# Performance work log

Hardware: AMD Instinct MI355X
Metric: run time of the kernel (lower is better)

The kernel has to match this reference:

```python
import jax, jax.numpy as jnp
import numpy as np

B, N, H, EMB, BOT = 32, 128, 64, 64, 64


def _node2edge(x):
    # x: (B, N, F) -> edges (B, N*N, 2F); edge e=i*N+j holds [x[j] (receiver), x[i] (sender)]
    b, n, f = x.shape
    recv = jnp.broadcast_to(x[:, None, :, :], (b, n, n, f))  # varies with j
    send = jnp.broadcast_to(x[:, :, None, :], (b, n, n, f))  # varies with i
    return jnp.concatenate([recv, send], axis=-1).reshape(b, n * n, 2 * f)


def _edge2node(e, n):
    # e: (B, N*N, F); receiver of edge i*N+j is j -> sum over i; divide by FEATURE dim (faithful to source)
    b, _, f = e.shape
    return e.reshape(b, n, n, f).sum(axis=1) / f


def _lin(x, w, b):
    return x @ w + b


def setup_inputs() -> dict:
    key = jax.random.key(0)
    ks = jax.random.split(key, 24)

    def w(k, i, o):
        return jax.random.normal(k, (i, o), jnp.float32) / np.sqrt(i)

    def bias(k, o):
        return jax.random.normal(k, (o,), jnp.float32) * 0.01

    return {
        "h_states": jax.random.normal(ks[0], (B, N, H), jnp.float32),
        "end_pos": jax.random.normal(ks[1], (B, N, 2), jnp.float32),
        "se_w": w(ks[2], 2, EMB), "se_b": bias(ks[3], EMB),
        "s1_w": w(ks[4], 2 * H + EMB, 128), "s1_b": bias(ks[5], 128),
        "s2_w": w(ks[6], 128, H), "s2_b": bias(ks[7], H),
        "n1_w": w(ks[8], H, 128), "n1_b": bias(ks[9], 128),
        "n2_w": w(ks[10], 128, H), "n2_b": bias(ks[11], H),
        "e1_w": w(ks[12], 2 * H, 128), "e1_b": bias(ks[13], 128),
        "e2_w": w(ks[14], 128, H), "e2_b": bias(ks[15], H),
        "f1_w": w(ks[16], H, 128), "f1_b": bias(ks[17], 128),
        "f2_w": w(ks[18], 128, BOT), "f2_b": bias(ks[19], BOT),
    }


def reference(h_states, end_pos, se_w, se_b, s1_w, s1_b, s2_w, s2_b,
              n1_w, n1_b, n2_w, n2_b, e1_w, e1_b, e2_w, e2_b,
              f1_w, f1_b, f2_w, f2_b):
    b, n, _ = h_states.shape
    # relative positions: pos[i] - pos[j] for edge i*N+j -> (B, N*N, 2)
    rel_pos = (end_pos[:, :, None, :] - end_pos[:, None, :, :]).reshape(b, n * n, 2)
    rel_emb = _lin(rel_pos, se_w, se_b)  # (B, N*N, EMB)

    edge_feat = jnp.concatenate([_node2edge(h_states), rel_emb], axis=-1)  # (B, N*N, 2H+EMB)
    # nmp_mlp_start: two linears, no activation (activation=None), dropout inert in eval
    edge_feat = _lin(_lin(edge_feat, s1_w, s1_b), s2_w, s2_b)  # (B, N*N, H)

    # nmp_layers=2 -> one (node mlp, edge mlp) pair, no activations
    node_feat = _lin(_lin(_edge2node(edge_feat, n), n1_w, n1_b), n2_w, n2_b)
    edge_feat = _lin(_lin(_node2edge(node_feat), e1_w, e1_b), e2_w, e2_b)

    # nmp_mlp_end: Linear -> ReLU -> Linear -> ReLU
    x = _edge2node(edge_feat, n)
    x = jax.nn.relu(_lin(x, f1_w, f1_b))
    x = jax.nn.relu(_lin(x, f2_w, f2_b))
    return x  # (B, N, BOT)
```

## Files before the change

### kernel.cpp

```cpp
#include <hip/hip_runtime.h>

enum : int {
  WS_A1  = 0,
  WS_B1  = 4096,
  WS_SE2 = 8192,
  WS_NW  = 12288,
  WS_D1  = 16384,
  WS_D2  = 20480,
  WS_K0  = 24576,
  WS_NB  = 24704,
  WS_D0  = 24768,
  WS_P1  = 24832,
  WS_P2  = 28928,
  WS_A2  = 37120,
  WS_K1  = 37248,
  WS_C2  = 37312,
  WS_H1  = 37440,
  WS_H2  = 45632,
  WS_H3  = 45888,
  WS_END = 49984
};

template<int N, int BS>
__device__ __forceinline__ void dot4row(const float* __restrict__ a, int as,
                                        const float* __restrict__ b, float c[4]){
  float c0=0.f,c1=0.f,c2=0.f,c3=0.f;
  #pragma unroll
  for (int k=0;k<N;++k){
    float bv = b[k*BS];
    c0 = fmaf(a[k],        bv, c0);
    c1 = fmaf(a[as+k],     bv, c1);
    c2 = fmaf(a[2*as+k],   bv, c2);
    c3 = fmaf(a[3*as+k],   bv, c3);
  }
  c[0]=c0;c[1]=c1;c[2]=c2;c[3]=c3;
}

template<int N, int BS>
__device__ __forceinline__ float dot1(const float* __restrict__ a, const float* __restrict__ b){
  float c = 0.f;
  #pragma unroll
  for (int k=0;k<N;++k) c = fmaf(a[k], b[k*BS], c);
  return c;
}

__global__ __launch_bounds__(256) void k_lvl0(
    const float* __restrict__ se_b,
    const float* __restrict__ s1_w, const float* __restrict__ s1_b,
    const float* __restrict__ s2_w,
    const float* __restrict__ n1_w, const float* __restrict__ n1_b,
    const float* __restrict__ n2_w, const float* __restrict__ n2_b,
    const float* __restrict__ e1_w, const float* __restrict__ e1_b,
    const float* __restrict__ e2_w, const float* __restrict__ e2_b,
    float* __restrict__ ws)
{
  int blk = blockIdx.x, t = threadIdx.x;
  if (blk < 24) {
    int which = blk >> 2, lb = blk & 3;
    int col = t & 63, row = lb * 16 + (t >> 6) * 4;
    const float* a; const float* b; float* o;
    switch (which) {
      case 0: a = s1_w + row * 128;         b = s2_w + col; o = ws + WS_A1;  break;
      case 1: a = s1_w + (64 + row) * 128;  b = s2_w + col; o = ws + WS_B1;  break;
      case 2: a = s1_w + (128 + row) * 128; b = s2_w + col; o = ws + WS_SE2; break;
      case 3: a = n1_w + row * 128;         b = n2_w + col; o = ws + WS_NW;  break;
      case 4: a = e1_w + row * 128;         b = e2_w + col; o = ws + WS_D1;  break;
      default:a = e1_w + (64 + row) * 128;  b = e2_w + col; o = ws + WS_D2;  break;
    }
    float c[4];
    dot4row<128, 64>(a, 128, b, c);
    #pragma unroll
    for (int i = 0; i < 4; ++i) o[(row + i) * 64 + col] = c[i];
  } else {
    if (t < 128) {
      ws[WS_K0 + t] = dot1<64, 128>(se_b, s1_w + 128 * 128 + t) + s1_b[t];
    } else if (t < 192) {
      int c = t - 128;
      ws[WS_NB + c] = dot1<128, 64>(n1_b, n2_w + c) + n2_b[c];
    } else {
      int c = t - 192;
      ws[WS_D0 + c] = 2.f * (dot1<128, 64>(e1_b, e2_w + c) + e2_b[c]);
    }
  }
}

__global__ __launch_bounds__(256) void k_lvl1(
    const float* __restrict__ se_w, const float* __restrict__ s2_w,
    const float* __restrict__ f1_w, float* __restrict__ ws)
{
  int blk = blockIdx.x, t = threadIdx.x;
  if (blk < 4) {
    int col = t & 63, row = blk * 16 + (t >> 6) * 4;
    float c[4];
    dot4row<64, 64>(ws + WS_A1 + row * 64, 64, ws + WS_NW + col, c);
    #pragma unroll
    for (int i = 0; i < 4; ++i) ws[WS_P1 + (row + i) * 64 + col] = c[i];
  } else if (blk < 12) {
    int c128 = t & 127, row = (blk - 4) * 8 + (t >> 7) * 4;
    float c[4];
    dot4row<64, 128>(ws + WS_D1 + row * 64, 64, f1_w + c128, c);
    #pragma unroll
    for (int i = 0; i < 4; ++i) ws[WS_P2 + (row + i) * 128 + c128] = c[i];
  } else {
    __shared__ float sA2[128];
    if (t < 128) {
      int r = t >> 6, c = t & 63;
      float v = dot1<64, 64>(se_w + r * 64, ws + WS_SE2 + c);
      sA2[t] = v;
      ws[WS_A2 + t] = v;
    } else if (t < 192) {
      int c = t - 128;
      ws[WS_K1 + c] = dot1<128, 64>(ws + WS_K0, s2_w + c);
    }
    __syncthreads();
    if (t < 128) {
      int r = t >> 6, c = t & 63;
      ws[WS_C2 + t] = -2.f * dot1<64, 64>(sA2 + r * 64, ws + WS_NW + c);
    }
  }
}

__global__ __launch_bounds__(256) void k_lvl2(
    const float* __restrict__ h, const float* __restrict__ pos,
    const float* __restrict__ s2_b, const float* __restrict__ f1_w,
    const float* __restrict__ f1_b, float* __restrict__ ws)
{
  int blk = blockIdx.x, t = threadIdx.x;
  if (blk < 8) {
    int c128 = t & 127, row = blk * 8 + (t >> 7) * 4;
    float c[4];
    dot4row<64, 128>(ws + WS_P1 + row * 64, 64, ws + WS_P2 + c128, c);
    #pragma unroll
    for (int i = 0; i < 4; ++i) ws[WS_H1 + (row + i) * 128 + c128] = 4.f * c[i];
    return;
  }
  if (blk == 8) {
    int r = t >> 7, c = t & 127;
    ws[WS_H2 + t] = 2.f * dot1<64, 128>(ws + WS_C2 + r * 64, ws + WS_P2 + c);
    return;
  }
  __shared__ float sX[64], sP[2], sv[64], sc3[64], sN[64], sg3[64], part[256];
  int b = blk - 9;
  { int k = t & 63, g = t >> 6; float s = 0.f;
    #pragma unroll 8
    for (int j = g * 32; j < g * 32 + 32; ++j) s += h[(b * 128 + j) * 64 + k];
    part[t] = s; }
  __syncthreads();
  if (t < 64) sX[t] = (part[t] + part[64 + t]) + (part[128 + t] + part[192 + t]);
  else if (t < 66) { int cc = t - 64; float s = 0.f;
    #pragma unroll 16
    for (int j = 0; j < 128; ++j) s += pos[(b * 128 + j) * 2 + cc];
    sP[cc] = s; }
  __syncthreads();
  if (t < 64) {
    float acc = dot1<64, 64>(sX, ws + WS_B1 + t);
    acc += sP[0] * ws[WS_A2 + t] + sP[1] * ws[WS_A2 + 64 + t];
    sv[t] = acc * (1.f / 64.f) + 2.f * ws[WS_K1 + t] + 2.f * s2_b[t];
  }
  __syncthreads();
  if (t < 64) {
    sc3[t] = dot1<64, 64>(sv, ws + WS_NW + t) + ws[WS_NB + t];
  }
  __syncthreads();
  if (t < 64) {
    float acc = 2.f * dot1<64, 64>(sX, ws + WS_P1 + t);
    sN[t] = acc + sP[0] * ws[WS_C2 + t] + sP[1] * ws[WS_C2 + 64 + t] + 128.f * sc3[t];
  }
  __syncthreads();
  if (t < 64) {
    float a1 = dot1<64, 64>(sc3, ws + WS_D1 + t);
    float a2 = dot1<64, 64>(sN, ws + WS_D2 + t);
    sg3[t] = 2.f * a1 + a2 * (1.f / 64.f) + ws[WS_D0 + t];
  }
  __syncthreads();
  if (t < 128) {
    ws[WS_H3 + b * 128 + t] = dot1<64, 128>(sg3, f1_w + t) + f1_b[t];
  }
}

__global__ __launch_bounds__(256) void k_main(
    const float* __restrict__ h, const float* __restrict__ pos,
    const float* __restrict__ f2_w, const float* __restrict__ f2_b,
    const float* __restrict__ ws, float* __restrict__ out)
{
  __shared__ __align__(16) float lH1[64 * 128];
  __shared__ __align__(16) float lH2[2 * 128];
  __shared__ float lh3[128], lf2b[64];
  __shared__ __align__(16) float lx[16 * 64];
  __shared__ float lp[16 * 2];
  __shared__ __align__(16) float lh1[16 * 128];
  int blk = blockIdx.x, t = threadIdx.x;
  int b = blk >> 3, j0 = (blk & 7) * 16;
  for (int i = t; i < 2048; i += 256) ((float4*)lH1)[i] = ((const float4*)(ws + WS_H1))[i];
  for (int i = t; i < 64; i += 256) ((float4*)lH2)[i] = ((const float4*)(ws + WS_H2))[i];
  if (t < 128) lh3[t] = ws[WS_H3 + b * 128 + t];
  if (t < 64) lf2b[t] = f2_b[t];
  { ((float4*)lx)[t] = ((const float4*)(h + (size_t)(b * 128 + j0) * 64))[t]; }
  if (t < 32) lp[t] = pos[(b * 128 + j0) * 2 + t];
  __syncthreads();
  {
    int d = t & 127, g = t >> 7, n0 = g * 8;
    float acc[8];
    #pragma unroll
    for (int i = 0; i < 8; ++i)
      acc[i] = lh3[d] + lp[(n0 + i) * 2] * lH2[d] + lp[(n0 + i) * 2 + 1] * lH2[128 + d];
    #pragma unroll 4
    for (int k = 0; k < 64; k += 4) {
      float h0 = lH1[k * 128 + d], h1v = lH1[(k + 1) * 128 + d],
            h2v = lH1[(k + 2) * 128 + d], h3v = lH1[(k + 3) * 128 + d];
      #pragma unroll
      for (int i = 0; i < 8; ++i) {
        float4 xv = *(const float4*)&lx[(n0 + i) * 64 + k];
        acc[i] = fmaf(xv.x, h0, fmaf(xv.y, h1v, fmaf(xv.z, h2v, fmaf(xv.w, h3v, acc[i]))));
      }
    }
    #pragma unroll
    for (int i = 0; i < 8; ++i) lh1[(n0 + i) * 128 + d] = fmaxf(acc[i], 0.f);
  }
  __syncthreads();
  {
    int d = t & 63, g = t >> 6, n0 = g * 4;
    float acc[4];
    #pragma unroll
    for (int i = 0; i < 4; ++i) acc[i] = lf2b[d];
    #pragma unroll 4
    for (int k = 0; k < 128; k += 4) {
      float f0 = f2_w[k * 64 + d], f1v = f2_w[(k + 1) * 64 + d],
            f2v = f2_w[(k + 2) * 64 + d], f3v = f2_w[(k + 3) * 64 + d];
      #pragma unroll
      for (int i = 0; i < 4; ++i) {
        float4 hv = *(const float4*)&lh1[(n0 + i) * 128 + k];
        acc[i] = fmaf(hv.x, f0, fmaf(hv.y, f1v, fmaf(hv.z, f2v, fmaf(hv.w, f3v, acc[i]))));
      }
    }
    #pragma unroll
    for (int i = 0; i < 4; ++i)
      out[(size_t)(b * 128 + j0 + n0 + i) * 64 + d] = fmaxf(acc[i], 0.f);
  }
}

extern "C" void kernel_launch(void* const* d_in, const int* in_sizes, int n_in,
                              void* d_out, int out_size, void* d_ws, size_t ws_size,
                              hipStream_t stream) {
  const float* h    = (const float*)d_in[0];
  const float* pos  = (const float*)d_in[1];
  const float* se_w = (const float*)d_in[2];
  const float* se_b = (const float*)d_in[3];
  const float* s1_w = (const float*)d_in[4];
  const float* s1_b = (const float*)d_in[5];
  const float* s2_w = (const float*)d_in[6];
  const float* s2_b = (const float*)d_in[7];
  const float* n1_w = (const float*)d_in[8];
  const float* n1_b = (const float*)d_in[9];
  const float* n2_w = (const float*)d_in[10];
  const float* n2_b = (const float*)d_in[11];
  const float* e1_w = (const float*)d_in[12];
  const float* e1_b = (const float*)d_in[13];
  const float* e2_w = (const float*)d_in[14];
  const float* e2_b = (const float*)d_in[15];
  const float* f1_w = (const float*)d_in[16];
  const float* f1_b = (const float*)d_in[17];
  const float* f2_w = (const float*)d_in[18];
  const float* f2_b = (const float*)d_in[19];
  float* ws = (float*)d_ws;
  float* out = (float*)d_out;

  hipLaunchKernelGGL(k_lvl0, dim3(25), dim3(256), 0, stream,
                     se_b, s1_w, s1_b, s2_w, n1_w, n1_b, n2_w, n2_b,
                     e1_w, e1_b, e2_w, e2_b, ws);
  hipLaunchKernelGGL(k_lvl1, dim3(13), dim3(256), 0, stream, se_w, s2_w, f1_w, ws);
  hipLaunchKernelGGL(k_lvl2, dim3(41), dim3(256), 0, stream, h, pos, s2_b, f1_w, f1_b, ws);
  hipLaunchKernelGGL(k_main, dim3(256), dim3(256), 0, stream, h, pos, f2_w, f2_b, ws, out);
}
```

Baseline: 32.91 us.

## Collapse three weight-folding launches into one prep kernel via vector chains

Replaces the three dependent precompute kernels with a single kernel. The first 32 blocks build the folded H1/H2 weight products column by column, each as a chain of matrix-vector products through the weights. The remaining 32 blocks compute the per-batch H3 vector by propagating through the layers directly instead of using precomposed 64x64 products. This removes two kernel launches and their dependency bubbles, at the cost of more serial per-block work and uncoalesced weight reads (threads stride rows of e2_w/n2_w/s2_w/e1_w/n1_w/s1_w) within each block.

```diff
diff --git a/kernel.cpp b/kernel.cpp
--- a/kernel.cpp
+++ b/kernel.cpp
@@ -1,180 +1,184 @@
 #include <hip/hip_runtime.h>
 
 enum : int {
-  WS_A1  = 0,
-  WS_B1  = 4096,
-  WS_SE2 = 8192,
-  WS_NW  = 12288,
-  WS_D1  = 16384,
-  WS_D2  = 20480,
-  WS_K0  = 24576,
-  WS_NB  = 24704,
-  WS_D0  = 24768,
-  WS_P1  = 24832,
-  WS_P2  = 28928,
-  WS_A2  = 37120,
-  WS_K1  = 37248,
-  WS_C2  = 37312,
-  WS_H1  = 37440,
-  WS_H2  = 45632,
-  WS_H3  = 45888,
-  WS_END = 49984
+  WS_H1 = 0,
+  WS_H2 = 8192,
+  WS_H3 = 8448,
+  WS_END = 12544
 };
 
-template<int N, int BS>
-__device__ __forceinline__ void dot4row(const float* __restrict__ a, int as,
-                                        const float* __restrict__ b, float c[4]){
-  float c0=0.f,c1=0.f,c2=0.f,c3=0.f;
-  #pragma unroll
-  for (int k=0;k<N;++k){
-    float bv = b[k*BS];
-    c0 = fmaf(a[k],        bv, c0);
-    c1 = fmaf(a[as+k],     bv, c1);
-    c2 = fmaf(a[2*as+k],   bv, c2);
-    c3 = fmaf(a[3*as+k],   bv, c3);
-  }
-  c[0]=c0;c[1]=c1;c[2]=c2;c[3]=c3;
-}
-
-template<int N, int BS>
-__device__ __forceinline__ float dot1(const float* __restrict__ a, const float* __restrict__ b){
-  float c = 0.f;
-  #pragma unroll
-  for (int k=0;k<N;++k) c = fmaf(a[k], b[k*BS], c);
-  return c;
-}
-
-__global__ __launch_bounds__(256) void k_lvl0(
-    const float* __restrict__ se_b,
+__global__ __launch_bounds__(256) void k_prep(
+    const float* __restrict__ h, const float* __restrict__ pos,
+    const float* __restrict__ se_w, const float* __restrict__ se_b,
     const float* __restrict__ s1_w, const float* __restrict__ s1_b,
-    const float* __restrict__ s2_w,
+    const float* __restrict__ s2_w, const float* __restrict__ s2_b,
     const float* __restrict__ n1_w, const float* __restrict__ n1_b,
     const float* __restrict__ n2_w, const float* __restrict__ n2_b,
     const float* __restrict__ e1_w, const float* __restrict__ e1_b,
     const float* __restrict__ e2_w, const float* __restrict__ e2_b,
+    const float* __restrict__ f1_w, const float* __restrict__ f1_b,
     float* __restrict__ ws)
 {
   int blk = blockIdx.x, t = threadIdx.x;
-  if (blk < 24) {
-    int which = blk >> 2, lb = blk & 3;
-    int col = t & 63, row = lb * 16 + (t >> 6) * 4;
-    const float* a; const float* b; float* o;
-    switch (which) {
-      case 0: a = s1_w + row * 128;         b = s2_w + col; o = ws + WS_A1;  break;
-      case 1: a = s1_w + (64 + row) * 128;  b = s2_w + col; o = ws + WS_B1;  break;
-      case 2: a = s1_w + (128 + row) * 128; b = s2_w + col; o = ws + WS_SE2; break;
-      case 3: a = n1_w + row * 128;         b = n2_w + col; o = ws + WS_NW;  break;
-      case 4: a = e1_w + row * 128;         b = e2_w + col; o = ws + WS_D1;  break;
-      default:a = e1_w + (64 + row) * 128;  b = e2_w + col; o = ws + WS_D2;  break;
-    }
-    float c[4];
-    dot4row<128, 64>(a, 128, b, c);
-    #pragma unroll
-    for (int i = 0; i < 4; ++i) o[(row + i) * 64 + col] = c[i];
+  if (blk < 32) {
+    __shared__ float wv[4][128];
+    __shared__ float uv[4][64];
+    int g = t >> 6, lane = t & 63, c = blk * 4 + g;
+    { float a0 = 0.f, a1 = 0.f;
+      #pragma unroll
+      for (int k = 0; k < 64; ++k) {
+        float f = f1_w[k * 128 + c];
+        a0 = fmaf(e2_w[lane * 64 + k], f, a0);
+        a1 = fmaf(e2_w[(lane + 64) * 64 + k], f, a1);
+      }
+      wv[g][lane] = a0; wv[g][lane + 64] = a1; }
+    __syncthreads();
+    { float a = 0.f;
+      #pragma unroll
+      for (int m = 0; m < 128; ++m) a = fmaf(e1_w[lane * 128 + m], wv[g][m], a);
+      uv[g][lane] = a; }
+    __syncthreads();
+    { float b0 = 0.f, b1 = 0.f;
+      #pragma unroll
+      for (int k = 0; k < 64; ++k) {
+        float u = uv[g][k];
+        b0 = fmaf(n2_w[lane * 64 + k], u, b0);
+        b1 = fmaf(n2_w[(lane + 64) * 64 + k], u, b1);
+      }
+      wv[g][lane] = b0; wv[g][lane + 64] = b1; }
+    __syncthreads();
+    { float a = 0.f;
+      #pragma unroll
+      for (int m = 0; m < 128; ++m) a = fmaf(n1_w[lane * 128 + m], wv[g][m], a);
+      uv[g][lane] = a; }
+    __syncthreads();
+    { float b0 = 0.f, b1 = 0.f;
+      #pragma unroll
+      for (int k = 0; k < 64; ++k) {
+        float u = uv[g][k];
+        b0 = fmaf(s2_w[lane * 64 + k], u, b0);
+        b1 = fmaf(s2_w[(lane + 64) * 64 + k], u, b1);
+      }
+      wv[g][lane] = b0; wv[g][lane + 64] = b1; }
+    __syncthreads();
+    { float a = 0.f, z = 0.f;
+      #pragma unroll
+      for (int m = 0; m < 128; ++m) {
+        float w = wv[g][m];
+        a = fmaf(s1_w[lane * 128 + m], w, a);
+        z = fmaf(s1_w[(128 + lane) * 128 + m], w, z);
+      }
+      ws[WS_H1 + lane * 128 + c] = 4.f * a;
+      float r0 = se_w[lane] * z, r1 = se_w[64 + lane] * z;
+      #pragma unroll
+      for (int m = 1; m < 64; m <<= 1) {
+        r0 += __shfl_xor(r0, m, 64);
+        r1 += __shfl_xor(r1, m, 64);
+      }
+      if (lane == 0) { ws[WS_H2 + c] = -4.f * r0; ws[WS_H2 + 128 + c] = -4.f * r1; } }
   } else {
-    if (t < 128) {
-      ws[WS_K0 + t] = dot1<64, 128>(se_b, s1_w + 128 * 128 + t) + s1_b[t];
-    } else if (t < 192) {
-      int c = t - 128;
-      ws[WS_NB + c] = dot1<128, 64>(n1_b, n2_w + c) + n2_b[c];
-    } else {
-      int c = t - 192;
-      ws[WS_D0 + c] = 2.f * (dot1<128, 64>(e1_b, e2_w + c) + e2_b[c]);
-    }
-  }
-}
-
-__global__ __launch_bounds__(256) void k_lvl1(
-    const float* __restrict__ se_w, const float* __restrict__ s2_w,
-    const float* __restrict__ f1_w, float* __restrict__ ws)
-{
-  int blk = blockIdx.x, t = threadIdx.x;
-  if (blk < 4) {
-    int col = t & 63, row = blk * 16 + (t >> 6) * 4;
-    float c[4];
-    dot4row<64, 64>(ws + WS_A1 + row * 64, 64, ws + WS_NW + col, c);
-    #pragma unroll
-    for (int i = 0; i < 4; ++i) ws[WS_P1 + (row + i) * 64 + col] = c[i];
-  } else if (blk < 12) {
-    int c128 = t & 127, row = (blk - 4) * 8 + (t >> 7) * 4;
-    float c[4];
-    dot4row<64, 128>(ws + WS_D1 + row * 64, 64, f1_w + c128, c);
-    #pragma unroll
-    for (int i = 0; i < 4; ++i) ws[WS_P2 + (row + i) * 128 + c128] = c[i];
-  } else {
-    __shared__ float sA2[128];
-    if (t < 128) {
-      int r = t >> 6, c = t & 63;
-      float v = dot1<64, 64>(se_w + r * 64, ws + WS_SE2 + c);
-      sA2[t] = v;
-      ws[WS_A2 + t] = v;
-    } else if (t < 192) {
-      int c = t - 128;
-      ws[WS_K1 + c] = dot1<128, 64>(ws + WS_K0, s2_w + c);
-    }
-    __syncthreads();
-    if (t < 128) {
-      int r = t >> 6, c = t & 63;
-      ws[WS_C2 + t] = -2.f * dot1<64, 64>(sA2 + r * 64, ws + WS_NW + c);
-    }
-  }
-}
-
-__global__ __launch_bounds__(256) void k_lvl2(
-    const float* __restrict__ h, const float* __restrict__ pos,
-    const float* __restrict__ s2_b, const float* __restrict__ f1_w,
-    const float* __restrict__ f1_b, float* __restrict__ ws)
-{
-  int blk = blockIdx.x, t = threadIdx.x;
-  if (blk < 8) {
-    int c128 = t & 127, row = blk * 8 + (t >> 7) * 4;
-    float c[4];
-    dot4row<64, 128>(ws + WS_P1 + row * 64, 64, ws + WS_P2 + c128, c);
-    #pragma unroll
-    for (int i = 0; i < 4; ++i) ws[WS_H1 + (row + i) * 128 + c128] = 4.f * c[i];
-    return;
-  }
-  if (blk == 8) {
-    int r = t >> 7, c = t & 127;
-    ws[WS_H2 + t] = 2.f * dot1<64, 128>(ws + WS_C2 + r * 64, ws + WS_P2 + c);
-    return;
-  }
-  __shared__ float sX[64], sP[2], sv[64], sc3[64], sN[64], sg3[64], part[256];
-  int b = blk - 9;
-  { int k = t & 63, g = t >> 6; float s = 0.f;
-    #pragma unroll 8
-    for (int j = g * 32; j < g * 32 + 32; ++j) s += h[(b * 128 + j) * 64 + k];
-    part[t] = s; }
-  __syncthreads();
-  if (t < 64) sX[t] = (part[t] + part[64 + t]) + (part[128 + t] + part[192 + t]);
-  else if (t < 66) { int cc = t - 64; float s = 0.f;
-    #pragma unroll 16
-    for (int j = 0; j < 128; ++j) s += pos[(b * 128 + j) * 2 + cc];
-    sP[cc] = s; }
-  __syncthreads();
-  if (t < 64) {
-    float acc = dot1<64, 64>(sX, ws + WS_B1 + t);
-    acc += sP[0] * ws[WS_A2 + t] + sP[1] * ws[WS_A2 + 64 + t];
-    sv[t] = acc * (1.f / 64.f) + 2.f * ws[WS_K1 + t] + 2.f * s2_b[t];
-  }
-  __syncthreads();
-  if (t < 64) {
-    sc3[t] = dot1<64, 64>(sv, ws + WS_NW + t) + ws[WS_NB + t];
-  }
-  __syncthreads();
-  if (t < 64) {
-    float acc = 2.f * dot1<64, 64>(sX, ws + WS_P1 + t);
-    sN[t] = acc + sP[0] * ws[WS_C2 + t] + sP[1] * ws[WS_C2 + 64 + t] + 128.f * sc3[t];
-  }
-  __syncthreads();
-  if (t < 64) {
-    float a1 = dot1<64, 64>(sc3, ws + WS_D1 + t);
-    float a2 = dot1<64, 64>(sN, ws + WS_D2 + t);
-    sg3[t] = 2.f * a1 + a2 * (1.f / 64.f) + ws[WS_D0 + t];
-  }
-  __syncthreads();
-  if (t < 128) {
-    ws[WS_H3 + b * 128 + t] = dot1<64, 128>(sg3, f1_w + t) + f1_b[t];
+    int b = blk - 32;
+    __shared__ float part[256], sX[64], sP[2];
+    __shared__ float L0[128], L1[128], L2[128], L3[128], M0[64], M1[64];
+    { int k = t & 63, g = t >> 6; float s = 0.f;
+      #pragma unroll 8
+      for (int j = g * 32; j < g * 32 + 32; ++j) s += h[(b * 128 + j) * 64 + k];
+      part[t] = s; }
+    __syncthreads();
+    if (t < 64) sX[t] = (part[t] + part[64 + t]) + (part[128 + t] + part[192 + t]);
+    else if (t < 66) { int cc = t - 64; float s = 0.f;
+      #pragma unroll 16
+      for (int j = 0; j < 128; ++j) s += pos[(b * 128 + j) * 2 + cc];
+      sP[cc] = s; }
+    __syncthreads();
+    { int g = t >> 7, o = t & 127;
+      if (g == 0) {
+        float a = 0.f, kk = 0.f;
+        #pragma unroll
+        for (int k = 0; k < 64; ++k) {
+          a  = fmaf(sX[k],   s1_w[k * 128 + o],        a);
+          kk = fmaf(se_b[k], s1_w[(128 + k) * 128 + o], kk);
+        }
+        L0[o] = a; L1[o] = kk + s1_b[o];
+      } else {
+        float p0 = sP[0], p1 = sP[1];
+        float a = 0.f, yy = 0.f;
+        #pragma unroll
+        for (int k = 0; k < 64; ++k) {
+          a = fmaf(sX[k], s1_w[(64 + k) * 128 + o], a);
+          float qk = fmaf(p1, se_w[64 + k], p0 * se_w[k]);
+          yy = fmaf(qk, s1_w[(128 + k) * 128 + o], yy);
+        }
+        L2[o] = a; L3[o] = yy;
+      } }
+    __syncthreads();
+    if (t < 128) { int g = t >> 6, c = t & 63;
+      float a = 0.f;
+      if (g == 0) {
+        #pragma unroll
+        for (int o = 0; o < 128; ++o) {
+          float r2 = fmaf(2.f, L1[o], (L2[o] + L3[o]) * (1.f / 64.f));
+          a = fmaf(r2, s2_w[o * 64 + c], a);
+        }
+        M0[c] = a + 2.f * s2_b[c];
+      } else {
+        #pragma unroll
+        for (int o = 0; o < 128; ++o)
+          a = fmaf(2.f * (L0[o] - L3[o]), s2_w[o * 64 + c], a);
+        M1[c] = a;
+      } }
+    __syncthreads();
+    { int g = t >> 7, o = t & 127;
+      float a = 0.f;
+      if (g == 0) {
+        #pragma unroll
+        for (int k = 0; k < 64; ++k) a = fmaf(M0[k], n1_w[k * 128 + o], a);
+        L0[o] = a + n1_b[o];
+      } else {
+        #pragma unroll
+        for (int k = 0; k < 64; ++k) a = fmaf(M1[k], n1_w[k * 128 + o], a);
+        L1[o] = a;
+      } }
+    __syncthreads();
+    if (t < 128) { int g = t >> 6, c = t & 63;
+      float a = 0.f;
+      if (g == 0) {
+        #pragma unroll
+        for (int o = 0; o < 128; ++o) a = fmaf(L0[o], n2_w[o * 64 + c], a);
+        M0[c] = a + n2_b[c];
+      } else {
+        #pragma unroll
+        for (int o = 0; o < 128; ++o) a = fmaf(L1[o], n2_w[o * 64 + c], a);
+        M1[c] = a;
+      } }
+    __syncthreads();
+    { int g = t >> 7, o = t & 127;
+      float a = 0.f;
+      if (g == 0) {
+        #pragma unroll
+        for (int k = 0; k < 64; ++k) a = fmaf(M0[k], e1_w[k * 128 + o], a);
+        L0[o] = a;
+      } else {
+        #pragma unroll
+        for (int k = 0; k < 64; ++k) {
+          float nb = fmaf(128.f, M0[k], M1[k]);
+          a = fmaf(nb, e1_w[(64 + k) * 128 + o], a);
+        }
+        L1[o] = a;
+      } }
+    __syncthreads();
+    if (t < 64) { float a = 0.f;
+      #pragma unroll
+      for (int o = 0; o < 128; ++o) {
+        float gv = fmaf(L1[o], (1.f / 64.f), fmaf(2.f, L0[o], 2.f * e1_b[o]));
+        a = fmaf(gv, e2_w[o * 64 + t], a);
+      }
+      M0[t] = a + 2.f * e2_b[t]; }
+    __syncthreads();
+    if (t < 128) { float a = 0.f;
+      #pragma unroll
+      for (int k = 0; k < 64; ++k) a = fmaf(M0[k], f1_w[k * 128 + t], a);
+      ws[WS_H3 + b * 128 + t] = a + f1_b[t]; }
   }
 }
 
@@ -265,10 +269,9 @@
   float* ws = (float*)d_ws;
   float* out = (float*)d_out;
 
-  hipLaunchKernelGGL(k_lvl0, dim3(25), dim3(256), 0, stream,
-                     se_b, s1_w, s1_b, s2_w, n1_w, n1_b, n2_w, n2_b,
-                     e1_w, e1_b, e2_w, e2_b, ws);
-  hipLaunchKernelGGL(k_lvl1, dim3(13), dim3(256), 0, stream, se_w, s2_w, f1_w, ws);
-  hipLaunchKernelGGL(k_lvl2, dim3(41), dim3(256), 0, stream, h, pos, s2_b, f1_w, f1_b, ws);
+  hipLaunchKernelGGL(k_prep, dim3(64), dim3(256), 0, stream,
+                     h, pos, se_w, se_b, s1_w, s1_b, s2_w, s2_b,
+                     n1_w, n1_b, n2_w, n2_b, e1_w, e1_b, e2_w, e2_b,
+                     f1_w, f1_b, ws);
   hipLaunchKernelGGL(k_main, dim3(256), dim3(256), 0, stream, h, pos, f2_w, f2_b, ws, out);
 }
```

New measurement: 41.61 us. 1.26x slower.
